# Kernel optimization log

Hardware: AMD Instinct MI355X
Metric: run time of the kernel (lower is better)

## Reference

```python
import jax, jax.numpy as jnp
import numpy as np

B, L, D, V = 2, 512, 512, 32000
TRAIN_FRAC = 0.01
LOSS_WEIGHTS = (1.0, 0.25)  # (forward branch, backward_ar_loss_weight)


def _make_pairs():
    # cartesian_prod(arange(L), arange(L)) filtered by bi - fi >= 2, then random subsample
    fi_g, bi_g = np.meshgrid(np.arange(L), np.arange(L), indexing='ij')
    fi_all, bi_all = fi_g.ravel(), bi_g.ravel()
    valid = (bi_all - fi_all) >= 2
    fi_all, bi_all = fi_all[valid], bi_all[valid]
    num_pairs = fi_all.shape[0]
    n_sub = max(int(num_pairs * TRAIN_FRAC), 1)
    perm = np.random.default_rng(0).permutation(num_pairs)[:n_sub]
    return jnp.asarray(fi_all[perm], jnp.int32), jnp.asarray(bi_all[perm], jnp.int32)


def setup_inputs() -> dict:
    key = jax.random.key(0)
    k_fe, k_be, k_seq, k_w1, k_w2 = jax.random.split(key, 5)
    fi, bi = _make_pairs()  # [N], N = 1303
    return {
        'forward_embeds': jax.random.normal(k_fe, (B, L, D), jnp.float32),
        'backward_embeds': jax.random.normal(k_be, (B, L, D), jnp.float32),
        'seq': jax.random.randint(k_seq, (B, L), 0, V, dtype=jnp.int32),
        'fi': fi,
        'bi': bi,
        'w1': jax.random.normal(k_w1, (2 * D, D), jnp.float32) * 0.02,
        'b1': jnp.zeros((D,), jnp.float32),
        'w2': jax.random.normal(k_w2, (D, 2 * V), jnp.float32) * 0.02,
        'b2': jnp.zeros((2 * V,), jnp.float32),
    }


def reference(forward_embeds, backward_embeds, seq, fi, bi, w1, b1, w2, b2):
    # gather fwd/bwd embeddings at the (fi, bi) pair indices and concat: [B, N, 2D]
    fb_embeds = jnp.concatenate([forward_embeds[:, fi], backward_embeds[:, bi]], axis=-1)
    # text head: Linear(2D->D) -> LeakyReLU(0.01) -> Linear(D->2V)
    h = jax.nn.leaky_relu(jnp.einsum('bne,ed->bnd', fb_embeds, w1) + b1)
    logits = jnp.einsum('bnd,dv->bnv', h, w2) + b2  # [B, N, 2V]
    n = logits.shape[1]
    # (fb l) layout: first V classes = forward branch, last V = backward branch
    logp = jax.nn.log_softmax(logits.reshape(B, n, 2, V), axis=-1)  # [B, N, 2, V]
    # NOTE: source computes labels_fi = fi + 1 but actually indexes seq at fi/bi
    labels = jnp.stack([seq[:, fi], seq[:, bi]], axis=-1)  # [B, N, 2]
    nll = -jnp.take_along_axis(logp, labels[..., None], axis=-1)[..., 0]  # [B, N, 2]
    w = jnp.asarray(LOSS_WEIGHTS, logits.dtype)  # per-branch loss weights
    return (nll * w).mean()
```

## Files before the change

### kernel.cpp

```cpp
#include <hip/hip_runtime.h>


typedef __bf16 bf16x8 __attribute__((ext_vector_type(8)));
typedef __bf16 bf16x4 __attribute__((ext_vector_type(4)));
typedef float f32x4  __attribute__((ext_vector_type(4)));

#define MFMA16(a, b, c) __builtin_amdgcn_mfma_f32_16x16x32_bf16(a, b, c, 0, 0, 0)

static constexpr int Bsz   = 2;
static constexpr int L     = 512;
static constexpr int D     = 512;
static constexpr int V     = 32000;
static constexpr int K1    = 2 * D;
static constexpr int N1    = D;
static constexpr int K2    = D;
static constexpr int N2    = 2 * V;
static constexpr int NSTRIP = N2 / 64;

__device__ __host__ inline size_t apack_chunk(int panel, int ks, int mi) {
    return (((size_t)panel * 16 + ks) * 4 + mi) * 512;
}

__global__ void prep_kernel(const float* __restrict__ fwd,
                            const float* __restrict__ bwd,
                            const int* __restrict__ fi,
                            const int* __restrict__ bi,
                            const int* __restrict__ seq,
                            const float* __restrict__ w1,
                            __bf16* __restrict__ A1,
                            __bf16* __restrict__ W1T,
                            int* __restrict__ labcol,
                            float* __restrict__ out,
                            int N, int M, int Mpad, int G1) {
    __shared__ __align__(16) __bf16 tile[64][68];
    if ((int)blockIdx.x >= G1) {
        int bid = blockIdx.x - G1;
        int bx = bid & 7, by = bid >> 3;
        int t  = threadIdx.x;
        int tx = t & 15, ty = t >> 4;
        int n0 = bx * 64, k0 = by * 64;
        for (int i = 0; i < 4; i++) {
            int k = k0 + ty + 16 * i;
            float4 v = *(const float4*)(w1 + (size_t)k * N1 + n0 + tx * 4);
            tile[tx * 4 + 0][ty + 16 * i] = (__bf16)v.x;
            tile[tx * 4 + 1][ty + 16 * i] = (__bf16)v.y;
            tile[tx * 4 + 2][ty + 16 * i] = (__bf16)v.z;
            tile[tx * 4 + 3][ty + 16 * i] = (__bf16)v.w;
        }
        __syncthreads();
        for (int i = 0; i < 4; i++) {
            int n = n0 + ty + 16 * i;
            bf16x4 o;
            o[0] = tile[ty + 16 * i][tx * 4 + 0];
            o[1] = tile[ty + 16 * i][tx * 4 + 1];
            o[2] = tile[ty + 16 * i][tx * 4 + 2];
            o[3] = tile[ty + 16 * i][tx * 4 + 3];
            *(bf16x4*)(W1T + (size_t)n * K1 + k0 + tx * 4) = o;
        }
        return;
    }
    int t = blockIdx.x * 256 + threadIdx.x;
    if (t == 0) *out = 0.0f;
    if (t < Mpad * 2) {
        int m = t >> 1, br = t & 1;
        if (m >= M) labcol[m * 2 + br] = -1;
        else {
            int b = m / N, n = m - b * N;
            int tok = br ? seq[b * L + bi[n]] : seq[b * L + fi[n]];
            labcol[m * 2 + br] = br * V + tok;
        }
    }
    int total = Mpad * (K1 / 8);
    if (t >= total) return;
    int m  = t >> 7;
    int c8 = (t & 127) * 8;
    bf16x8 out8;
    if (m < M) {
        int b = m / N;
        int n = m - b * N;
        const float* src;
        if (c8 < D) src = fwd + ((size_t)(b * L + fi[n])) * D + c8;
        else        src = bwd + ((size_t)(b * L + bi[n])) * D + (c8 - D);
        float4 v0 = *(const float4*)(src);
        float4 v1 = *(const float4*)(src + 4);
        out8[0] = (__bf16)v0.x; out8[1] = (__bf16)v0.y;
        out8[2] = (__bf16)v0.z; out8[3] = (__bf16)v0.w;
        out8[4] = (__bf16)v1.x; out8[5] = (__bf16)v1.y;
        out8[6] = (__bf16)v1.z; out8[7] = (__bf16)v1.w;
    } else {
        for (int j = 0; j < 8; j++) out8[j] = (__bf16)0.0f;
    }
    *(bf16x8*)(A1 + (size_t)m * K1 + c8) = out8;
}

__global__ __launch_bounds__(256) void gemm1_kernel(
        const __bf16* __restrict__ A, const __bf16* __restrict__ Bt,
        const float* __restrict__ bias, __bf16* __restrict__ Apack, int K) {
    __shared__ __align__(16) __bf16 At[128][40];
    __shared__ __align__(16) __bf16 Bl[128][40];
    __shared__ __align__(16) __bf16 Cld[128][136];
    const int t = threadIdx.x;
    const int by = blockIdx.y, bx = blockIdx.x;
    const int m0 = by * 128, n0 = bx * 128;
    const int srow = t >> 2, schunk = (t & 3) * 8;
    const int wave = t >> 6, lane = t & 63;
    const int wrow = (wave >> 1) * 64, wcol = (wave & 1) * 64;
    const int q = lane >> 4, ln = lane & 15;

    bf16x8 rA0 = *(const bf16x8*)(A  + (size_t)(m0 + srow)      * K + schunk);
    bf16x8 rA1 = *(const bf16x8*)(A  + (size_t)(m0 + srow + 64) * K + schunk);
    bf16x8 rB0 = *(const bf16x8*)(Bt + (size_t)(n0 + srow)      * K + schunk);
    bf16x8 rB1 = *(const bf16x8*)(Bt + (size_t)(n0 + srow + 64) * K + schunk);

    f32x4 acc[4][4] = {};
    for (int k0 = 0; k0 < K; k0 += 32) {
        __syncthreads();
        *(bf16x8*)&At[srow][schunk]      = rA0;
        *(bf16x8*)&At[srow + 64][schunk] = rA1;
        *(bf16x8*)&Bl[srow][schunk]      = rB0;
        *(bf16x8*)&Bl[srow + 64][schunk] = rB1;
        __syncthreads();
        if (k0 + 32 < K) {
            int kn = k0 + 32 + schunk;
            rA0 = *(const bf16x8*)(A  + (size_t)(m0 + srow)      * K + kn);
            rA1 = *(const bf16x8*)(A  + (size_t)(m0 + srow + 64) * K + kn);
            rB0 = *(const bf16x8*)(Bt + (size_t)(n0 + srow)      * K + kn);
            rB1 = *(const bf16x8*)(Bt + (size_t)(n0 + srow + 64) * K + kn);
        }
        bf16x8 af[4], bfr[4];
        for (int i = 0; i < 4; i++) af[i]  = *(const bf16x8*)&At[wrow + i * 16 + ln][q * 8];
        for (int i = 0; i < 4; i++) bfr[i] = *(const bf16x8*)&Bl[wcol + i * 16 + ln][q * 8];
        for (int mi = 0; mi < 4; mi++)
            for (int ni = 0; ni < 4; ni++)
                acc[mi][ni] = MFMA16(af[mi], bfr[ni], acc[mi][ni]);
    }
    for (int ni = 0; ni < 4; ni++) {
        int gcol = n0 + wcol + ni * 16 + ln;
        float bv = bias[gcol];
        for (int mi = 0; mi < 4; mi++)
            for (int r = 0; r < 4; r++) {
                float v = acc[mi][ni][r] + bv;
                v = v > 0.0f ? v : 0.01f * v;
                Cld[wrow + mi * 16 + q * 4 + r][wcol + ni * 16 + ln] = (__bf16)v;
            }
    }
    __syncthreads();
    for (int i = 0; i < 8; i++) {
        int c   = wave + 4 * i;
        int pl  = c >> 4, ksl = (c >> 2) & 3, mi = c & 3;
        int row = pl * 64 + mi * 16 + (lane & 15);
        int col = ksl * 32 + (lane >> 4) * 8;
        bf16x8 v = *(const bf16x8*)&Cld[row][col];
        size_t base = apack_chunk(2 * by + pl, 4 * bx + ksl, mi);
        *(bf16x8*)(Apack + base + lane * 8) = v;
    }
}

__global__ __launch_bounds__(512, 4) void gemm2_kernel(
        const __bf16* __restrict__ Apack, const float* __restrict__ w2,
        const float* __restrict__ b2, const int* __restrict__ labcol,
        float* __restrict__ partial, float* __restrict__ lab, int Mpad) {
    __shared__ __align__(16) __bf16 Bp[64 * 512];
    const int t = threadIdx.x;
    const int strip = blockIdx.x;
    const int c0 = strip * 64;
    const int branch = (c0 >= V) ? 1 : 0;

    {
        const int col = t & 63;
        const int ni = col >> 4, lncol = col & 15;
        const int kb0 = (t >> 6) * 8;
        for (int r = 0; r < 8; r++) {
            int kb = kb0 + r * 64;
            int ks = kb >> 5, qk = (kb >> 3) & 3;
            float v[8];
#pragma unroll
            for (int j = 0; j < 8; j++)
                v[j] = __builtin_nontemporal_load(w2 + (size_t)(kb + j) * N2 + c0 + col);
            bf16x8 o;
#pragma unroll
            for (int j = 0; j < 8; j++) o[j] = (__bf16)v[j];
            *(bf16x8*)&Bp[(size_t)(((ks * 4 + ni) * 64 + qk * 16 + lncol)) * 8] = o;
        }
    }
    __syncthreads();

    const int wave = t >> 6, lane = t & 63;
    const int q = lane >> 4, ln = lane & 15;

    float bvn[4];
#pragma unroll
    for (int ni = 0; ni < 4; ni++) bvn[ni] = b2[c0 + ni * 16 + ln];

    const int npanels = Mpad >> 6;
    for (int p = wave; p < npanels; p += 8) {
        const __bf16* base = Apack + apack_chunk(p, 0, 0) + lane * 8;

        f32x4 acc[4][4] = {};
        bf16x8 afc[4], afn[4];
#pragma unroll
        for (int mi = 0; mi < 4; mi++)
            afc[mi] = *(const bf16x8*)(base + mi * 512);
#pragma unroll 1
        for (int ks = 0; ks < 16; ks++) {
            if (ks < 15) {
#pragma unroll
                for (int mi = 0; mi < 4; mi++)
                    afn[mi] = *(const bf16x8*)(base + (size_t)(ks + 1) * 2048 + mi * 512);
            }
            bf16x8 bf[4];
#pragma unroll
            for (int ni = 0; ni < 4; ni++)
                bf[ni] = *(const bf16x8*)&Bp[(size_t)(ks * 4 + ni) * 512 + lane * 8];
#pragma unroll
            for (int mi = 0; mi < 4; mi++)
#pragma unroll
                for (int ni = 0; ni < 4; ni++)
                    acc[mi][ni] = MFMA16(afc[mi], bf[ni], acc[mi][ni]);
#pragma unroll
            for (int mi = 0; mi < 4; mi++) afc[mi] = afn[mi];
        }

        int lc[4][4];
#pragma unroll
        for (int mi = 0; mi < 4; mi++)
#pragma unroll
            for (int r = 0; r < 4; r++)
                lc[mi][r] = labcol[(p * 64 + mi * 16 + q * 4 + r) * 2 + branch];

        float rowsum[4][4];
#pragma unroll
        for (int mi = 0; mi < 4; mi++)
#pragma unroll
            for (int r = 0; r < 4; r++) rowsum[mi][r] = 0.0f;

#pragma unroll
        for (int ni = 0; ni < 4; ni++) {
            const int gcol = c0 + ni * 16 + ln;
            const float bv = bvn[ni];
#pragma unroll
            for (int mi = 0; mi < 4; mi++)
#pragma unroll
                for (int r = 0; r < 4; r++) {
                    float v = acc[mi][ni][r] + bv;
                    rowsum[mi][r] += __expf(v);
                    if (gcol == lc[mi][r]) {
                        int gm = p * 64 + mi * 16 + q * 4 + r;
                        lab[gm * 2 + branch] = v;
                    }
                }
        }
#pragma unroll
        for (int mi = 0; mi < 4; mi++)
#pragma unroll
            for (int r = 0; r < 4; r++) {
                float s = rowsum[mi][r];
                s += __shfl_xor(s, 1);
                s += __shfl_xor(s, 2);
                s += __shfl_xor(s, 4);
                s += __shfl_xor(s, 8);
                rowsum[mi][r] = s;
            }
        float mine = 0.0f;
        const int srcl = ((lane >> 2) & 3) * 16;
#pragma unroll
        for (int mi2 = 0; mi2 < 4; mi2++)
#pragma unroll
            for (int r2 = 0; r2 < 4; r2++) {
                float tv = __shfl(rowsum[mi2][r2], srcl);
                if ((lane >> 4) == mi2 && (lane & 3) == r2) mine = tv;
            }
        partial[(size_t)strip * Mpad + p * 64 + lane] = mine;
    }
}

__global__ __launch_bounds__(256) void final_kernel(
        const float* __restrict__ partial, const float* __restrict__ lab,
        float* __restrict__ out, int M, int Mpad) {
    __shared__ float red[4][64];
    const int br = blockIdx.x & 1;
    const int m0 = (blockIdx.x >> 1) * 64;
    const int wave = threadIdx.x >> 6, lane = threadIdx.x & 63;
    const int s0 = br * (NSTRIP / 2) + wave * (NSTRIP / 8);
    float s = 0.0f;
#pragma unroll 5
    for (int i = 0; i < NSTRIP / 8; i++)
        s += partial[(size_t)(s0 + i) * Mpad + m0 + lane];
    red[wave][lane] = s;
    __syncthreads();
    if (wave == 0) {
        float tot = red[0][lane] + red[1][lane] + red[2][lane] + red[3][lane];
        int m = m0 + lane;
        float acc = 0.0f;
        if (m < M)
            acc = (br ? 0.25f : 1.0f) * (logf(tot) - lab[m * 2 + br]);
        acc += __shfl_xor(acc, 32);
        acc += __shfl_xor(acc, 16);
        acc += __shfl_xor(acc, 8);
        acc += __shfl_xor(acc, 4);
        acc += __shfl_xor(acc, 2);
        acc += __shfl_xor(acc, 1);
        if (lane == 0) atomicAdd(out, acc / (float)(2 * M));
    }
}

extern "C" void kernel_launch(void* const* d_in, const int* in_sizes, int n_in,
                              void* d_out, int out_size, void* d_ws, size_t ws_size,
                              hipStream_t stream) {
    const float* fwd = (const float*)d_in[0];
    const float* bwd = (const float*)d_in[1];
    const int*   seq = (const int*)d_in[2];
    const int*   fi  = (const int*)d_in[3];
    const int*   bi  = (const int*)d_in[4];
    const float* w1  = (const float*)d_in[5];
    const float* b1  = (const float*)d_in[6];
    const float* w2  = (const float*)d_in[7];
    const float* b2  = (const float*)d_in[8];
    float* out = (float*)d_out;

    const int N    = in_sizes[3];
    const int M    = Bsz * N;
    const int Mpad = ((M + 255) / 256) * 256;

    char* ws = (char*)d_ws;
    __bf16* A1    = (__bf16*)(ws);
    __bf16* W1T   = (__bf16*)(ws + (size_t)Mpad * K1 * 2);
    __bf16* Apack = (__bf16*)((char*)W1T + (size_t)N1 * K1 * 2);
    float*  partial = (float*)((char*)Apack + (size_t)Mpad * N1 * 2);
    float*  lab     = (float*)((char*)partial + (size_t)NSTRIP * Mpad * 4);
    int*    labcol  = (int*)((char*)lab + (size_t)Mpad * 2 * 4);

    {
        int G1 = Mpad * (K1 / 8) / 256;
        prep_kernel<<<G1 + 128, 256, 0, stream>>>(
            fwd, bwd, fi, bi, seq, w1, A1, W1T, labcol, out, N, M, Mpad, G1);
    }
    gemm1_kernel<<<dim3(N1 / 128, Mpad / 128), 256, 0, stream>>>(A1, W1T, b1, Apack, K1);
    gemm2_kernel<<<NSTRIP, 512, 0, stream>>>(Apack, w2, b2, labcol, partial, lab, Mpad);
    final_kernel<<<(Mpad / 64) * 2, 256, 0, stream>>>(partial, lab, out, M, Mpad);
}
```

Baseline: 394.1 us.

## Switch vocab GEMM to 32x32x16 MFMA with repacked A/B fragment layouts

Replaces the 16x16x32 bf16 MFMA tiles in the second GEMM with 32x32x16 MFMA. The packed hidden-activation layout written by the first GEMM changes to match, as does the LDS layout of the W2 strip. The log-sum-exp epilogue is rewritten for the 32x32 accumulator register mapping, with one extra xor-shuffle stage and a new row-sum redistribution. The goal is fewer LDS fragment loads and MFMA instructions per FLOP. The cost is larger accumulator vectors and more shuffles in the epilogue, which may raise register pressure under the 512-thread, 4-block launch bound.

```diff
diff --git a/kernel.cpp b/kernel.cpp
--- a/kernel.cpp
+++ b/kernel.cpp
@@ -4,8 +4,10 @@
 typedef __bf16 bf16x8 __attribute__((ext_vector_type(8)));
 typedef __bf16 bf16x4 __attribute__((ext_vector_type(4)));
 typedef float f32x4  __attribute__((ext_vector_type(4)));
+typedef float f32x16 __attribute__((ext_vector_type(16)));
 
 #define MFMA16(a, b, c) __builtin_amdgcn_mfma_f32_16x16x32_bf16(a, b, c, 0, 0, 0)
+#define MFMA32(a, b, c) __builtin_amdgcn_mfma_f32_32x32x16_bf16(a, b, c, 0, 0, 0)
 
 static constexpr int Bsz   = 2;
 static constexpr int L     = 512;
@@ -17,8 +19,8 @@
 static constexpr int N2    = 2 * V;
 static constexpr int NSTRIP = N2 / 64;
 
-__device__ __host__ inline size_t apack_chunk(int panel, int ks, int mi) {
-    return (((size_t)panel * 16 + ks) * 4 + mi) * 512;
+__device__ __host__ inline size_t apack_chunk(int panel, int ks, int sub, int bi2) {
+    return ((((size_t)panel * 16 + ks) * 2 + sub) * 2 + bi2) * 512;
 }
 
 __global__ void prep_kernel(const float* __restrict__ fwd,
@@ -147,11 +149,11 @@
     __syncthreads();
     for (int i = 0; i < 8; i++) {
         int c   = wave + 4 * i;
-        int pl  = c >> 4, ksl = (c >> 2) & 3, mi = c & 3;
-        int row = pl * 64 + mi * 16 + (lane & 15);
-        int col = ksl * 32 + (lane >> 4) * 8;
+        int pl  = c >> 4, ksl = (c >> 2) & 3, sub = (c >> 1) & 1, bi2 = c & 1;
+        int row = pl * 64 + bi2 * 32 + (lane & 31);
+        int col = ksl * 32 + sub * 16 + (lane >> 5) * 8;
         bf16x8 v = *(const bf16x8*)&Cld[row][col];
-        size_t base = apack_chunk(2 * by + pl, 4 * bx + ksl, mi);
+        size_t base = apack_chunk(2 * by + pl, 4 * bx + ksl, sub, bi2);
         *(bf16x8*)(Apack + base + lane * 8) = v;
     }
 }
@@ -168,11 +170,11 @@
 
     {
         const int col = t & 63;
-        const int ni = col >> 4, lncol = col & 15;
+        const int bj2 = col >> 5, colh = col & 31;
         const int kb0 = (t >> 6) * 8;
         for (int r = 0; r < 8; r++) {
             int kb = kb0 + r * 64;
-            int ks = kb >> 5, qk = (kb >> 3) & 3;
+            int ks = kb >> 5, sub = (kb >> 4) & 1, ko = (kb >> 3) & 1;
             float v[8];
 #pragma unroll
             for (int j = 0; j < 8; j++)
@@ -180,96 +182,104 @@
             bf16x8 o;
 #pragma unroll
             for (int j = 0; j < 8; j++) o[j] = (__bf16)v[j];
-            *(bf16x8*)&Bp[(size_t)(((ks * 4 + ni) * 64 + qk * 16 + lncol)) * 8] = o;
+            *(bf16x8*)&Bp[(size_t)((((ks * 2 + sub) * 2 + bj2) * 64) + ko * 32 + colh) * 8] = o;
         }
     }
     __syncthreads();
 
     const int wave = t >> 6, lane = t & 63;
-    const int q = lane >> 4, ln = lane & 15;
-
-    float bvn[4];
-#pragma unroll
-    for (int ni = 0; ni < 4; ni++) bvn[ni] = b2[c0 + ni * 16 + ln];
+    const int h = lane >> 5, cl = lane & 31;
+
+    float bv2[2];
+#pragma unroll
+    for (int bj2 = 0; bj2 < 2; bj2++) bv2[bj2] = b2[c0 + bj2 * 32 + cl];
+
+    const int rlt  = lane & 31;
+    const int regt = (rlt & 3) + 4 * (rlt >> 3);
+    const int hnt  = (rlt >> 2) & 1;
 
     const int npanels = Mpad >> 6;
     for (int p = wave; p < npanels; p += 8) {
-        const __bf16* base = Apack + apack_chunk(p, 0, 0) + lane * 8;
-
-        f32x4 acc[4][4] = {};
-        bf16x8 afc[4], afn[4];
-#pragma unroll
-        for (int mi = 0; mi < 4; mi++)
-            afc[mi] = *(const bf16x8*)(base + mi * 512);
+        const __bf16* base = Apack + apack_chunk(p, 0, 0, 0) + lane * 8;
+
+        f32x16 acc[2][2] = {};
+        bf16x8 afc[2][2], afn[2][2];
+#pragma unroll
+        for (int sub = 0; sub < 2; sub++)
+#pragma unroll
+            for (int bi2 = 0; bi2 < 2; bi2++)
+                afc[sub][bi2] = *(const bf16x8*)(base + (size_t)(sub * 2 + bi2) * 512);
 #pragma unroll 1
         for (int ks = 0; ks < 16; ks++) {
             if (ks < 15) {
 #pragma unroll
-                for (int mi = 0; mi < 4; mi++)
-                    afn[mi] = *(const bf16x8*)(base + (size_t)(ks + 1) * 2048 + mi * 512);
-            }
-            bf16x8 bf[4];
-#pragma unroll
-            for (int ni = 0; ni < 4; ni++)
-                bf[ni] = *(const bf16x8*)&Bp[(size_t)(ks * 4 + ni) * 512 + lane * 8];
-#pragma unroll
-            for (int mi = 0; mi < 4; mi++)
-#pragma unroll
-                for (int ni = 0; ni < 4; ni++)
-                    acc[mi][ni] = MFMA16(afc[mi], bf[ni], acc[mi][ni]);
-#pragma unroll
-            for (int mi = 0; mi < 4; mi++) afc[mi] = afn[mi];
-        }
-
-        int lc[4][4];
-#pragma unroll
-        for (int mi = 0; mi < 4; mi++)
-#pragma unroll
-            for (int r = 0; r < 4; r++)
-                lc[mi][r] = labcol[(p * 64 + mi * 16 + q * 4 + r) * 2 + branch];
-
-        float rowsum[4][4];
-#pragma unroll
-        for (int mi = 0; mi < 4; mi++)
-#pragma unroll
-            for (int r = 0; r < 4; r++) rowsum[mi][r] = 0.0f;
-
-#pragma unroll
-        for (int ni = 0; ni < 4; ni++) {
-            const int gcol = c0 + ni * 16 + ln;
-            const float bv = bvn[ni];
-#pragma unroll
-            for (int mi = 0; mi < 4; mi++)
-#pragma unroll
-                for (int r = 0; r < 4; r++) {
-                    float v = acc[mi][ni][r] + bv;
-                    rowsum[mi][r] += __expf(v);
-                    if (gcol == lc[mi][r]) {
-                        int gm = p * 64 + mi * 16 + q * 4 + r;
+                for (int sub = 0; sub < 2; sub++)
+#pragma unroll
+                    for (int bi2 = 0; bi2 < 2; bi2++)
+                        afn[sub][bi2] = *(const bf16x8*)(base + (size_t)(((ks + 1) * 2 + sub) * 2 + bi2) * 512);
+            }
+            bf16x8 bfr[2][2];
+#pragma unroll
+            for (int sub = 0; sub < 2; sub++)
+#pragma unroll
+                for (int bj2 = 0; bj2 < 2; bj2++)
+                    bfr[sub][bj2] = *(const bf16x8*)&Bp[(size_t)((ks * 2 + sub) * 2 + bj2) * 512 + lane * 8];
+#pragma unroll
+            for (int sub = 0; sub < 2; sub++)
+#pragma unroll
+                for (int bi2 = 0; bi2 < 2; bi2++)
+#pragma unroll
+                    for (int bj2 = 0; bj2 < 2; bj2++)
+                        acc[bi2][bj2] = MFMA32(afc[sub][bi2], bfr[sub][bj2], acc[bi2][bj2]);
+#pragma unroll
+            for (int sub = 0; sub < 2; sub++)
+#pragma unroll
+                for (int bi2 = 0; bi2 < 2; bi2++)
+                    afc[sub][bi2] = afn[sub][bi2];
+        }
+
+        float mine = 0.0f;
+#pragma unroll
+        for (int bi2 = 0; bi2 < 2; bi2++) {
+            int lc16[16];
+#pragma unroll
+            for (int reg = 0; reg < 16; reg++)
+                lc16[reg] = labcol[(p * 64 + bi2 * 32 + (reg & 3) + 8 * (reg >> 2) + 4 * h) * 2 + branch];
+
+            float rs[16];
+#pragma unroll
+            for (int reg = 0; reg < 16; reg++) rs[reg] = 0.0f;
+
+#pragma unroll
+            for (int bj2 = 0; bj2 < 2; bj2++) {
+                const int gcol = c0 + bj2 * 32 + cl;
+                const float bv = bv2[bj2];
+#pragma unroll
+                for (int reg = 0; reg < 16; reg++) {
+                    float v = acc[bi2][bj2][reg] + bv;
+                    rs[reg] += __expf(v);
+                    if (gcol == lc16[reg]) {
+                        int gm = p * 64 + bi2 * 32 + (reg & 3) + 8 * (reg >> 2) + 4 * h;
                         lab[gm * 2 + branch] = v;
                     }
                 }
-        }
-#pragma unroll
-        for (int mi = 0; mi < 4; mi++)
-#pragma unroll
-            for (int r = 0; r < 4; r++) {
-                float s = rowsum[mi][r];
+            }
+#pragma unroll
+            for (int reg = 0; reg < 16; reg++) {
+                float s = rs[reg];
                 s += __shfl_xor(s, 1);
                 s += __shfl_xor(s, 2);
                 s += __shfl_xor(s, 4);
                 s += __shfl_xor(s, 8);
-                rowsum[mi][r] = s;
-            }
-        float mine = 0.0f;
-        const int srcl = ((lane >> 2) & 3) * 16;
-#pragma unroll
-        for (int mi2 = 0; mi2 < 4; mi2++)
-#pragma unroll
-            for (int r2 = 0; r2 < 4; r2++) {
-                float tv = __shfl(rowsum[mi2][r2], srcl);
-                if ((lane >> 4) == mi2 && (lane & 3) == r2) mine = tv;
-            }
+                s += __shfl_xor(s, 16);
+                rs[reg] = s;
+            }
+#pragma unroll
+            for (int reg = 0; reg < 16; reg++) {
+                float tv = __shfl(rs[reg], hnt * 32 + cl);
+                if ((lane >> 5) == bi2 && regt == reg) mine = tv;
+            }
+        }
         partial[(size_t)strip * Mpad + p * 64 + lane] = mine;
     }
 }
```

Result: slower. 429.7 us (+9.0%).
